# Optimization experiments

Hardware: AMD Instinct MI355X
Metric: run time of the kernel (lower is better)

## Reference

```python
import jax, jax.numpy as jnp
import numpy as np

N, IN_DIM, HID, OUT, E = 20000, 1024, 512, 128, 160000


def _xavier(key, fan_out, fan_in):
    a = (6.0 / (fan_in + fan_out)) ** 0.5
    return jax.random.uniform(key, (fan_out, fan_in), jnp.float32, -a, a)


def setup_inputs() -> dict:
    key = jax.random.key(0)
    ks = jax.random.split(key, 8)
    features = jax.random.normal(ks[0], (N, IN_DIM), jnp.float32)
    edge_index = jax.random.randint(ks[1], (2, E), 0, N, jnp.int64)
    W1 = _xavier(ks[2], HID, IN_DIM)   # conv1.lin.weight [out,in]
    b1 = jnp.zeros((HID,), jnp.float32)
    W2 = _xavier(ks[3], OUT, HID)      # conv2.lin.weight
    b2 = jnp.zeros((OUT,), jnp.float32)
    b3 = jnp.zeros((HID,), jnp.float32)  # conv3 bias (weight tied = W2.T)
    b4 = jnp.zeros((IN_DIM,), jnp.float32)  # conv4 bias (weight tied = W1.T)
    head1 = _xavier(ks[4], OUT, OUT)
    return dict(features=features, edge_index=edge_index, W1=W1, b1=b1,
                W2=W2, b2=b2, b3=b3, b4=b4, head1=head1)


def _gcn_conv(x, W, b, src, dst, norm, n):
    # GCNConv: transform then symmetric-normalized neighbor aggregation
    h = x @ W.T                       # [N, out]
    msg = h[src] * norm[:, None]      # [E', out] gathered + scaled
    out = jax.ops.segment_sum(msg, dst, num_segments=n)
    return out + b


def reference(features, edge_index, W1, b1, W2, b2, b3, b4, head1):
    n = features.shape[0]
    loops = jnp.arange(n, dtype=edge_index.dtype)
    src = jnp.concatenate([edge_index[0], loops])  # add self-loops
    dst = jnp.concatenate([edge_index[1], loops])
    deg = jax.ops.segment_sum(jnp.ones_like(dst, dtype=features.dtype), dst,
                              num_segments=n)
    dinv = jnp.where(deg > 0, deg ** -0.5, 0.0)
    norm = dinv[src] * dinv[dst]

    h1 = _gcn_conv(features, W1, b1, src, dst, norm, n)
    h2 = _gcn_conv(h1, W2, b2, src, dst, norm, n)
    z = h2 @ head1
    # tied weights: conv3.W = W2^T, conv4.W = W1^T
    h3 = _gcn_conv(z, W2.T, b3, src, dst, norm, n)
    h4 = _gcn_conv(h3, W1.T, b4, src, dst, norm, n)
    return z, h2, h4
```

## Files before the change

kernel.cpp:

```cpp
#include <hip/hip_runtime.h>

typedef short   short8  __attribute__((ext_vector_type(8)));
typedef unsigned short ushort8 __attribute__((ext_vector_type(8)));
typedef unsigned short bf4     __attribute__((ext_vector_type(4)));
typedef float   floatx4 __attribute__((ext_vector_type(4)));

__device__ __forceinline__ float bf2f(unsigned short h) {
    unsigned int u = ((unsigned int)h) << 16;
    return __builtin_bit_cast(float, u);
}
__device__ __forceinline__ unsigned short f2bf(float f) {
    unsigned int u = __builtin_bit_cast(unsigned int, f);
    u += 0x7fffu + ((u >> 16) & 1u);
    return (unsigned short)(u >> 16);
}


__global__ __launch_bounds__(256) void k_detect_f32(const unsigned short* __restrict__ X,
                                                    int nPairs, int* __restrict__ flags) {
    int i = blockIdx.x * 256 + threadIdx.x;
    if (i < nPairs) {
        unsigned short w = X[2 * i];
        if ((w & 0x7F80u) == 0x7F80u) atomicOr(&flags[0], 1);
    }
}

__global__ __launch_bounds__(256) void k_detect_i32(const int* __restrict__ ei,
                                                    int E, int* __restrict__ flags) {
    int i = blockIdx.x * 256 + threadIdx.x;
    if (i < E) {
        if (ei[2 * i + 1] != 0) atomicOr(&flags[1], 1);
    }
}


__global__ __launch_bounds__(256) void k_cvt_f32(const void* __restrict__ in,
                                                 float* __restrict__ out, int n,
                                                 const int* __restrict__ flags) {
    int i = blockIdx.x * 256 + threadIdx.x;
    if (i < n)
        out[i] = flags[0] ? ((const float*)in)[i] : bf2f(((const unsigned short*)in)[i]);
}

__global__ __launch_bounds__(256) void k_cvt8(const void* __restrict__ in,
                                              unsigned short* __restrict__ out,
                                              long n8, const int* __restrict__ flags) {
    long i = (long)blockIdx.x * 256 + threadIdx.x;
    if (i >= n8) return;
    ushort8 o;
    if (flags[0]) {
        const floatx4* f = (const floatx4*)in + i * 2;
        floatx4 a = f[0], b = f[1];
#pragma unroll
        for (int j = 0; j < 4; j++) { o[j] = f2bf(a[j]); o[4 + j] = f2bf(b[j]); }
    } else {
        o = *((const ushort8*)in + i);
    }
    *((ushort8*)out + i) = o;
}

__global__ __launch_bounds__(256) void k_tcvt(const void* __restrict__ in,
                                              unsigned short* __restrict__ out,
                                              int R, int C, const int* __restrict__ flags) {
    int idx = blockIdx.x * 256 + threadIdx.x;
    if (idx >= R * C) return;
    int r = idx / C, c = idx - r * C;
    unsigned short v = flags[0] ? f2bf(((const float*)in)[idx])
                                : ((const unsigned short*)in)[idx];
    out[(long)c * R + r] = v;
}


__global__ __launch_bounds__(256) void k_count(const int* __restrict__ ei, int E, int n,
                                               const int* __restrict__ flags,
                                               int* __restrict__ deg) {
    int e = blockIdx.x * 256 + threadIdx.x;
    if (e >= E) return;
    int sh = (flags[1] == 0) ? 1 : 0;
    int d = ei[(long)(E + e) << sh];
    if ((unsigned)d < (unsigned)n) atomicAdd(&deg[d], 1);
}

__global__ __launch_bounds__(256) void k_dinv(const int* __restrict__ deg,
                                              float* __restrict__ dinv, int n) {
    int i = blockIdx.x * 256 + threadIdx.x;
    if (i < n) dinv[i] = rsqrtf((float)(deg[i] + 1));
}

__global__ __launch_bounds__(1024) void k_scan(const int* __restrict__ deg,
                                               int* __restrict__ row_start,
                                               int* __restrict__ cursor, int n) {
    __shared__ int sums[1024];
    int t = threadIdx.x;
    int CH = (n + 1 + 1023) / 1024;
    int base = t * CH;
    int s = 0;
    for (int i = 0; i < CH; i++) {
        int idx = base + i;
        if (idx < n) s += deg[idx];
    }
    sums[t] = s;
    __syncthreads();
    for (int off = 1; off < 1024; off <<= 1) {
        int v = (t >= off) ? sums[t - off] : 0;
        __syncthreads();
        if (t >= off) sums[t] += v;
        __syncthreads();
    }
    int run = (t > 0) ? sums[t - 1] : 0;
    for (int i = 0; i < CH; i++) {
        int idx = base + i;
        if (idx < n) {
            row_start[idx] = run;
            cursor[idx] = run;
            run += deg[idx];
        } else if (idx == n) {
            row_start[n] = run;
        }
    }
}

__global__ __launch_bounds__(256) void k_fill(const int* __restrict__ ei, int E, int n,
                                              const int* __restrict__ flags,
                                              int* __restrict__ cursor,
                                              int* __restrict__ csr) {
    int e = blockIdx.x * 256 + threadIdx.x;
    if (e >= E) return;
    int sh = (flags[1] == 0) ? 1 : 0;
    int s = ei[(long)e << sh];
    int d = ei[(long)(E + e) << sh];
    if ((unsigned)d >= (unsigned)n || (unsigned)s >= (unsigned)n) return;
    int p = atomicAdd(&cursor[d], 1);
    csr[p] = s;
}


template <int BM, int BN>
__global__ __launch_bounds__(256, (BN == 128 ? 3 : 4))
void gemm_nt(const unsigned short* __restrict__ A,
             const unsigned short* __restrict__ Bt,
             void* __restrict__ Cv, long coff,
             const float* __restrict__ bias,
             int M, int N, int K, int finalOut,
             const int* __restrict__ flags) {
    constexpr int BK = 32, LDT = 40;
    constexpr int JR = BN / 16;
    constexpr int SM = BM / 64;
    __shared__ unsigned short sA[2][BM * LDT];
    __shared__ unsigned short sB[2][BN * LDT];
    const bool of32 = finalOut && flags[0];
    const bool hasb = bias != nullptr;
    const int t = threadIdx.x;

    const int GX = gridDim.x;
    const int nwg = GX * gridDim.y;
    const int orig = blockIdx.y * GX + blockIdx.x;
    const int q8 = nwg >> 3, r8 = nwg & 7;
    const int xcd = orig & 7, cidx = orig >> 3;
    const int swz = (xcd < r8 ? xcd * (q8 + 1) : r8 * (q8 + 1) + (xcd - r8) * q8) + cidx;
    const int m0 = (swz / GX) * BM;
    const int n0 = (swz % GX) * BN;

    const int w = t >> 6;
    const int lane = t & 63;
    const int id = lane & 15;
    const int q = lane >> 4;

    floatx4 acc[SM][JR];
#pragma unroll
    for (int s = 0; s < SM; s++)
#pragma unroll
        for (int j = 0; j < JR; j++) acc[s][j] = (floatx4)0.0f;

    const int ar = t >> 2;
    const int ac = (t & 3) * 8;

    const unsigned short* pa0 = A + (long)min(m0 + ar, M - 1) * K + ac;
    const unsigned short* pa1 = (SM == 2)
        ? A + (long)min(m0 + ar + 64, M - 1) * K + ac : pa0;
    const unsigned short* pb0 = Bt + (long)min(n0 + ar, N - 1) * K + ac;
    const unsigned short* pb1 = (JR == 8)
        ? Bt + (long)min(n0 + ar + 64, N - 1) * K + ac : pb0;

    {
        ushort8 va0 = *(const ushort8*)(pa0);
        ushort8 va1; if (SM == 2) va1 = *(const ushort8*)(pa1);
        ushort8 vb0 = *(const ushort8*)(pb0);
        ushort8 vb1; if (JR == 8) vb1 = *(const ushort8*)(pb1);
        *(ushort8*)(sA[0] + ar * LDT + ac) = va0;
        if (SM == 2) *(ushort8*)(sA[0] + (ar + 64) * LDT + ac) = va1;
        *(ushort8*)(sB[0] + ar * LDT + ac) = vb0;
        if (JR == 8) *(ushort8*)(sB[0] + (ar + 64) * LDT + ac) = vb1;
        __syncthreads();
    }

    auto STEP = [&](int k0, const unsigned short* sAr, const unsigned short* sBr,
                    unsigned short* sAw, unsigned short* sBw, bool last) {
        ushort8 na0, na1, nb0, nb1;
        if (!last) {
            na0 = *(const ushort8*)(pa0 + k0 + BK);
            if (SM == 2) na1 = *(const ushort8*)(pa1 + k0 + BK);
            nb0 = *(const ushort8*)(pb0 + k0 + BK);
            if (JR == 8) nb1 = *(const ushort8*)(pb1 + k0 + BK);
        }
        short8 afrag[SM], bfrag[JR];
#pragma unroll
        for (int s = 0; s < SM; s++)
            afrag[s] = *(const short8*)(sAr + ((SM == 2 ? 32 * w + 16 * s : 16 * w) + id) * LDT + q * 8);
#pragma unroll
        for (int j = 0; j < JR; j++)
            bfrag[j] = *(const short8*)(sBr + (16 * j + id) * LDT + q * 8);
#pragma unroll
        for (int s = 0; s < SM; s++)
#pragma unroll
            for (int j = 0; j < JR; j++)
                acc[s][j] = __builtin_amdgcn_mfma_f32_16x16x32_bf16(
                    bfrag[j], afrag[s], acc[s][j], 0, 0, 0);
        if (!last) {
            *(ushort8*)(sAw + ar * LDT + ac) = na0;
            if (SM == 2) *(ushort8*)(sAw + (ar + 64) * LDT + ac) = na1;
            *(ushort8*)(sBw + ar * LDT + ac) = nb0;
            if (JR == 8) *(ushort8*)(sBw + (ar + 64) * LDT + ac) = nb1;
            __syncthreads();
        }
    };

    for (int k0 = 0; k0 < K; k0 += 2 * BK) {
        STEP(k0, sA[0], sB[0], sA[1], sB[1], false);
        STEP(k0 + BK, sA[1], sB[1], sA[0], sB[0], k0 + 2 * BK >= K);
    }

#pragma unroll
    for (int s = 0; s < SM; s++) {
        const int row = m0 + (SM == 2 ? 32 * w + 16 * s : 16 * w) + id;
        if (row < M) {
#pragma unroll
            for (int j = 0; j < JR; j++) {
                const int colb = n0 + 16 * j + 4 * q;
                floatx4 v = acc[s][j];
                if (hasb) v = v + *(const floatx4*)(bias + colb);
                const long off = coff + (long)row * N + colb;
                if (of32) {
                    *(floatx4*)((float*)Cv + off) = v;
                } else {
                    bf4 o;
#pragma unroll
                    for (int r = 0; r < 4; r++) o[r] = f2bf(v[r]);
                    *(bf4*)((unsigned short*)Cv + off) = o;
                }
            }
        }
    }
}


template <int D>
__global__ __launch_bounds__(256) void k_agg(const unsigned short* __restrict__ T,
                                             const int* __restrict__ rs,
                                             const int* __restrict__ csr,
                                             const float* __restrict__ dinv,
                                             const float* __restrict__ bias,
                                             unsigned short* __restrict__ O, int n) {
    constexpr int TPN = D / 8;
    constexpr int NPB = 256 / TPN;
    int lt = threadIdx.x % TPN;
    int node = blockIdx.x * NPB + threadIdx.x / TPN;
    if (node >= n) return;
    int off = lt * 8;
    float acc[8];
#pragma unroll
    for (int i = 0; i < 8; i++) acc[i] = 0.0f;
    int beg = rs[node], end = rs[node + 1];
    for (int j = beg; j < end; j++) {
        int s = csr[j];
        if ((unsigned)s >= (unsigned)n) continue;
        float wgt = dinv[s];
        ushort8 v = *(const ushort8*)(T + (long)s * D + off);
#pragma unroll
        for (int i = 0; i < 8; i++) acc[i] += wgt * bf2f(v[i]);
    }
    float di = dinv[node];
    ushort8 sv = *(const ushort8*)(T + (long)node * D + off);
    ushort8 o;
#pragma unroll
    for (int i = 0; i < 8; i++) {
        float r = di * (acc[i] + di * bf2f(sv[i])) + (bias ? bias[off + i] : 0.0f);
        o[i] = f2bf(r);
    }
    *(ushort8*)(O + (long)node * D + off) = o;
}


__global__ __launch_bounds__(256) void k_out(const unsigned short* __restrict__ z,
                                             const unsigned short* __restrict__ h2,
                                             void* __restrict__ out, int nOut,
                                             const int* __restrict__ flags) {
    int i = blockIdx.x * 256 + threadIdx.x;
    if (i >= 2 * nOut) return;
    unsigned short v = (i < nOut) ? z[i] : h2[i - nOut];
    if (flags[0]) ((float*)out)[i] = bf2f(v);
    else ((unsigned short*)out)[i] = v;
}


extern "C" void kernel_launch(void* const* d_in, const int* in_sizes, int n_in,
                              void* d_out, int out_size, void* d_ws, size_t ws_size,
                              hipStream_t stream) {
    const int IN  = in_sizes[7];
    const int HID = in_sizes[3];
    const int OUT = in_sizes[5];
    const int Nn  = in_sizes[0] / IN;
    const int E   = in_sizes[1] / 2;

    const void* X   = d_in[0];
    const int*  ei  = (const int*)d_in[1];
    const void* W1  = d_in[2];
    const void* b1  = d_in[3];
    const void* W2  = d_in[4];
    const void* b2  = d_in[5];
    const void* b3  = d_in[6];
    const void* b4  = d_in[7];
    const void* Hd1 = d_in[8];

    char* base = (char*)d_ws;
    size_t o = 0;
    auto carve = [&](size_t bytes) -> char* {
        char* p = base + o;
        o = (o + bytes + 255) & ~(size_t)255;
        return p;
    };
    int*   flags  = (int*)carve(2 * 4);
    int*   deg    = (int*)carve((size_t)Nn * 4);
    int*   rowst  = (int*)carve((size_t)(Nn + 1) * 4);
    int*   cursor = (int*)carve((size_t)Nn * 4);
    float* dinv   = (float*)carve((size_t)Nn * 4);
    int*   csr    = (int*)carve((size_t)E * 4);
    float* biasf  = (float*)carve((size_t)(HID + OUT + HID + IN) * 4);
    float* bc1 = biasf, *bc2 = biasf + HID, *bc3 = biasf + HID + OUT,
         *bc4 = biasf + HID + OUT + HID;
    unsigned short* W1t  = (unsigned short*)carve((size_t)IN * HID * 2);
    unsigned short* W2t  = (unsigned short*)carve((size_t)HID * OUT * 2);
    unsigned short* H1t  = (unsigned short*)carve((size_t)OUT * OUT * 2);
    unsigned short* W1c  = (unsigned short*)carve((size_t)HID * IN * 2);
    unsigned short* W2c  = (unsigned short*)carve((size_t)OUT * HID * 2);
    unsigned short* Xb   = (unsigned short*)carve((size_t)Nn * IN * 2);
    unsigned short* t1   = (unsigned short*)carve((size_t)Nn * HID * 2);
    unsigned short* h1   = (unsigned short*)carve((size_t)Nn * HID * 2);
    unsigned short* h3   = (unsigned short*)carve((size_t)Nn * HID * 2);
    unsigned short* t2   = (unsigned short*)carve((size_t)Nn * OUT * 2);
    unsigned short* h2ws = (unsigned short*)carve((size_t)Nn * OUT * 2);
    unsigned short* zws  = (unsigned short*)carve((size_t)Nn * OUT * 2);

    hipMemsetAsync(flags, 0, 8, stream);
    hipMemsetAsync(deg, 0, (size_t)Nn * 4, stream);
    int nPairs = 1 << 20;
    k_detect_f32<<<(nPairs + 255) / 256, 256, 0, stream>>>((const unsigned short*)X, nPairs, flags);
    k_detect_i32<<<(E + 255) / 256, 256, 0, stream>>>(ei, E, flags);

    k_cvt_f32<<<(HID + 255) / 256, 256, 0, stream>>>(b1, bc1, HID, flags);
    k_cvt_f32<<<(OUT + 255) / 256, 256, 0, stream>>>(b2, bc2, OUT, flags);
    k_cvt_f32<<<(HID + 255) / 256, 256, 0, stream>>>(b3, bc3, HID, flags);
    k_cvt_f32<<<(IN + 255) / 256, 256, 0, stream>>>(b4, bc4, IN, flags);

    k_tcvt<<<(HID * IN + 255) / 256, 256, 0, stream>>>(W1, W1t, HID, IN, flags);
    k_tcvt<<<(OUT * HID + 255) / 256, 256, 0, stream>>>(W2, W2t, OUT, HID, flags);
    k_tcvt<<<(OUT * OUT + 255) / 256, 256, 0, stream>>>(Hd1, H1t, OUT, OUT, flags);

    {
        long n8x = (long)Nn * IN / 8;
        k_cvt8<<<(int)((n8x + 255) / 256), 256, 0, stream>>>(X, Xb, n8x, flags);
        long n8w1 = (long)HID * IN / 8;
        k_cvt8<<<(int)((n8w1 + 255) / 256), 256, 0, stream>>>(W1, W1c, n8w1, flags);
        long n8w2 = (long)OUT * HID / 8;
        k_cvt8<<<(int)((n8w2 + 255) / 256), 256, 0, stream>>>(W2, W2c, n8w2, flags);
    }

    k_count<<<(E + 255) / 256, 256, 0, stream>>>(ei, E, Nn, flags, deg);
    k_dinv<<<(Nn + 255) / 256, 256, 0, stream>>>(deg, dinv, Nn);
    k_scan<<<1, 1024, 0, stream>>>(deg, rowst, cursor, Nn);
    k_fill<<<(E + 255) / 256, 256, 0, stream>>>(ei, E, Nn, flags, cursor, csr);

    dim3 blk(256);
    auto ggrid = [&](int Ncols, int bn, int bm) {
        return dim3((Ncols + bn - 1) / bn, (Nn + bm - 1) / bm);
    };
    const long h2Off = (long)Nn * OUT, h4Off = (long)Nn * OUT * 2;

    gemm_nt<128, 64><<<ggrid(HID, 64, 128), blk, 0, stream>>>(Xb, W1c, t1, 0, nullptr, Nn, HID, IN, 0, flags);
    k_agg<512><<<(Nn * 64 + 255) / 256, blk, 0, stream>>>(t1, rowst, csr, dinv, bc1, h1, Nn);

    gemm_nt<64, 64><<<ggrid(OUT, 64, 64), blk, 0, stream>>>(h1, W2c, t2, 0, nullptr, Nn, OUT, HID, 0, flags);
    k_agg<128><<<(Nn * 16 + 255) / 256, blk, 0, stream>>>(t2, rowst, csr, dinv, bc2, h2ws, Nn);

    gemm_nt<64, 64><<<ggrid(OUT, 64, 64), blk, 0, stream>>>(h2ws, H1t, zws, 0, nullptr, Nn, OUT, OUT, 0, flags);

    k_agg<128><<<(Nn * 16 + 255) / 256, blk, 0, stream>>>(zws, rowst, csr, dinv, nullptr, t2, Nn);
    gemm_nt<128, 64><<<ggrid(HID, 64, 128), blk, 0, stream>>>(t2, W2t, h3, 0, bc3, Nn, HID, OUT, 0, flags);

    k_agg<512><<<(Nn * 64 + 255) / 256, blk, 0, stream>>>(h3, rowst, csr, dinv, nullptr, t1, Nn);
    gemm_nt<128, 128><<<ggrid(IN, 128, 128), blk, 0, stream>>>(t1, W1t, d_out, h4Off, bc4, Nn, IN, HID, 1, flags);

    k_out<<<(2 * (int)h2Off + 255) / 256, blk, 0, stream>>>(zws, h2ws, d_out, (int)h2Off, flags);
}
```

Baseline: 546.0 us.

## Fuse input conversions into GEMM loads and outputs into producers; merge prologue kernels

The first GEMMs now read fp32 inputs directly and convert them to bf16 while staging into shared memory, so the separate full-matrix conversion of the features (20000x1024) and of W1/W2 is no longer needed. The z and h2 outputs are written straight from the GEMM and aggregation epilogues, which removes the final copy kernel. Detection, degree zeroing and the bias conversions are merged into fewer launches, and the weight transpose now goes through tiled shared memory. The cost is twice the global traffic per A tile in the first GEMM, plus extra branches and registers in the GEMM loop.

```diff
diff --git a/kernel.cpp b/kernel.cpp
--- a/kernel.cpp
+++ b/kernel.cpp
@@ -16,58 +16,65 @@
 }
 
 
-__global__ __launch_bounds__(256) void k_detect_f32(const unsigned short* __restrict__ X,
-                                                    int nPairs, int* __restrict__ flags) {
+__global__ __launch_bounds__(256) void k_detect(const unsigned short* __restrict__ X,
+                                                int nPairs, const int* __restrict__ ei,
+                                                int E, int n,
+                                                int* __restrict__ flags,
+                                                int* __restrict__ deg) {
     int i = blockIdx.x * 256 + threadIdx.x;
     if (i < nPairs) {
         unsigned short w = X[2 * i];
         if ((w & 0x7F80u) == 0x7F80u) atomicOr(&flags[0], 1);
     }
-}
-
-__global__ __launch_bounds__(256) void k_detect_i32(const int* __restrict__ ei,
-                                                    int E, int* __restrict__ flags) {
-    int i = blockIdx.x * 256 + threadIdx.x;
     if (i < E) {
         if (ei[2 * i + 1] != 0) atomicOr(&flags[1], 1);
     }
-}
-
-
-__global__ __launch_bounds__(256) void k_cvt_f32(const void* __restrict__ in,
-                                                 float* __restrict__ out, int n,
-                                                 const int* __restrict__ flags) {
+    if (i < n) deg[i] = 0;
+}
+
+
+__global__ __launch_bounds__(256) void k_cvtb(const void* __restrict__ b1,
+                                              const void* __restrict__ b2,
+                                              const void* __restrict__ b3,
+                                              const void* __restrict__ b4,
+                                              float* __restrict__ out,
+                                              int L1, int L2, int L3, int L4,
+                                              const int* __restrict__ flags) {
     int i = blockIdx.x * 256 + threadIdx.x;
-    if (i < n)
-        out[i] = flags[0] ? ((const float*)in)[i] : bf2f(((const unsigned short*)in)[i]);
-}
-
-__global__ __launch_bounds__(256) void k_cvt8(const void* __restrict__ in,
-                                              unsigned short* __restrict__ out,
-                                              long n8, const int* __restrict__ flags) {
-    long i = (long)blockIdx.x * 256 + threadIdx.x;
-    if (i >= n8) return;
-    ushort8 o;
-    if (flags[0]) {
-        const floatx4* f = (const floatx4*)in + i * 2;
-        floatx4 a = f[0], b = f[1];
-#pragma unroll
-        for (int j = 0; j < 4; j++) { o[j] = f2bf(a[j]); o[4 + j] = f2bf(b[j]); }
-    } else {
-        o = *((const ushort8*)in + i);
-    }
-    *((ushort8*)out + i) = o;
-}
+    int n = L1 + L2 + L3 + L4;
+    if (i >= n) return;
+    const void* src; int off;
+    if (i < L1)                { src = b1; off = i; }
+    else if (i < L1 + L2)      { src = b2; off = i - L1; }
+    else if (i < L1 + L2 + L3) { src = b3; off = i - L1 - L2; }
+    else                       { src = b4; off = i - L1 - L2 - L3; }
+    out[i] = flags[0] ? ((const float*)src)[off]
+                      : bf2f(((const unsigned short*)src)[off]);
+}
+
 
 __global__ __launch_bounds__(256) void k_tcvt(const void* __restrict__ in,
                                               unsigned short* __restrict__ out,
                                               int R, int C, const int* __restrict__ flags) {
-    int idx = blockIdx.x * 256 + threadIdx.x;
-    if (idx >= R * C) return;
-    int r = idx / C, c = idx - r * C;
-    unsigned short v = flags[0] ? f2bf(((const float*)in)[idx])
-                                : ((const unsigned short*)in)[idx];
-    out[(long)c * R + r] = v;
+    __shared__ unsigned short tl[32][40];
+    const int c0 = blockIdx.x * 32, r0 = blockIdx.y * 32;
+    const int tx = threadIdx.x & 31, ty = threadIdx.x >> 5;
+    const bool f32 = flags[0] != 0;
+#pragma unroll
+    for (int k = 0; k < 32; k += 8) {
+        int r = r0 + ty + k, c = c0 + tx;
+        unsigned short v = 0;
+        if (r < R && c < C)
+            v = f32 ? f2bf(((const float*)in)[(long)r * C + c])
+                    : ((const unsigned short*)in)[(long)r * C + c];
+        tl[ty + k][tx] = v;
+    }
+    __syncthreads();
+#pragma unroll
+    for (int k = 0; k < 32; k += 8) {
+        int c = c0 + ty + k, r = r0 + tx;
+        if (c < C && r < R) out[(long)c * R + r] = tl[tx][ty + k];
+    }
 }
 
 
@@ -135,11 +142,29 @@
 }
 
 
+__device__ __forceinline__ void ld_any(const void* base, long elem, bool f32,
+                                       ushort8& u, floatx4& f0, floatx4& f1) {
+    if (f32) {
+        const floatx4* p = (const floatx4*)((const float*)base + elem);
+        f0 = p[0]; f1 = p[1];
+    } else {
+        u = *(const ushort8*)((const unsigned short*)base + elem);
+    }
+}
+__device__ __forceinline__ ushort8 cv_any(bool f32, ushort8 u, floatx4 f0, floatx4 f1) {
+    if (!f32) return u;
+    ushort8 r;
+#pragma unroll
+    for (int j = 0; j < 4; j++) { r[j] = f2bf(f0[j]); r[4 + j] = f2bf(f1[j]); }
+    return r;
+}
+
 template <int BM, int BN>
 __global__ __launch_bounds__(256, (BN == 128 ? 3 : 4))
-void gemm_nt(const unsigned short* __restrict__ A,
-             const unsigned short* __restrict__ Bt,
+void gemm_nt(const void* __restrict__ A, int aMaybeF32,
+             const void* __restrict__ Bt, int bMaybeF32,
              void* __restrict__ Cv, long coff,
+             void* __restrict__ Cv2, long c2off,
              const float* __restrict__ bias,
              int M, int N, int K, int finalOut,
              const int* __restrict__ flags) {
@@ -148,7 +173,10 @@
     constexpr int SM = BM / 64;
     __shared__ unsigned short sA[2][BM * LDT];
     __shared__ unsigned short sB[2][BN * LDT];
-    const bool of32 = finalOut && flags[0];
+    const bool isf32 = flags[0] != 0;
+    const bool af32 = aMaybeF32 && isf32;
+    const bool bf32 = bMaybeF32 && isf32;
+    const bool of32 = finalOut && isf32;
     const bool hasb = bias != nullptr;
     const int t = threadIdx.x;
 
@@ -175,33 +203,37 @@
     const int ar = t >> 2;
     const int ac = (t & 3) * 8;
 
-    const unsigned short* pa0 = A + (long)min(m0 + ar, M - 1) * K + ac;
-    const unsigned short* pa1 = (SM == 2)
-        ? A + (long)min(m0 + ar + 64, M - 1) * K + ac : pa0;
-    const unsigned short* pb0 = Bt + (long)min(n0 + ar, N - 1) * K + ac;
-    const unsigned short* pb1 = (JR == 8)
-        ? Bt + (long)min(n0 + ar + 64, N - 1) * K + ac : pb0;
+    const long ea0 = (long)min(m0 + ar, M - 1) * K + ac;
+    const long ea1 = (SM == 2) ? (long)min(m0 + ar + 64, M - 1) * K + ac : ea0;
+    const long eb0 = (long)min(n0 + ar, N - 1) * K + ac;
+    const long eb1 = (JR == 8) ? (long)min(n0 + ar + 64, N - 1) * K + ac : eb0;
 
     {
-        ushort8 va0 = *(const ushort8*)(pa0);
-        ushort8 va1; if (SM == 2) va1 = *(const ushort8*)(pa1);
-        ushort8 vb0 = *(const ushort8*)(pb0);
-        ushort8 vb1; if (JR == 8) vb1 = *(const ushort8*)(pb1);
-        *(ushort8*)(sA[0] + ar * LDT + ac) = va0;
-        if (SM == 2) *(ushort8*)(sA[0] + (ar + 64) * LDT + ac) = va1;
-        *(ushort8*)(sB[0] + ar * LDT + ac) = vb0;
-        if (JR == 8) *(ushort8*)(sB[0] + (ar + 64) * LDT + ac) = vb1;
+        ushort8 u; floatx4 f0, f1;
+        ld_any(A, ea0, af32, u, f0, f1);
+        *(ushort8*)(sA[0] + ar * LDT + ac) = cv_any(af32, u, f0, f1);
+        if (SM == 2) {
+            ld_any(A, ea1, af32, u, f0, f1);
+            *(ushort8*)(sA[0] + (ar + 64) * LDT + ac) = cv_any(af32, u, f0, f1);
+        }
+        ld_any(Bt, eb0, bf32, u, f0, f1);
+        *(ushort8*)(sB[0] + ar * LDT + ac) = cv_any(bf32, u, f0, f1);
+        if (JR == 8) {
+            ld_any(Bt, eb1, bf32, u, f0, f1);
+            *(ushort8*)(sB[0] + (ar + 64) * LDT + ac) = cv_any(bf32, u, f0, f1);
+        }
         __syncthreads();
     }
 
     auto STEP = [&](int k0, const unsigned short* sAr, const unsigned short* sBr,
                     unsigned short* sAw, unsigned short* sBw, bool last) {
         ushort8 na0, na1, nb0, nb1;
+        floatx4 fa00, fa01, fa10, fa11, fb00, fb01, fb10, fb11;
         if (!last) {
-            na0 = *(const ushort8*)(pa0 + k0 + BK);
-            if (SM == 2) na1 = *(const ushort8*)(pa1 + k0 + BK);
-            nb0 = *(const ushort8*)(pb0 + k0 + BK);
-            if (JR == 8) nb1 = *(const ushort8*)(pb1 + k0 + BK);
+            ld_any(A, ea0 + k0 + BK, af32, na0, fa00, fa01);
+            if (SM == 2) ld_any(A, ea1 + k0 + BK, af32, na1, fa10, fa11);
+            ld_any(Bt, eb0 + k0 + BK, bf32, nb0, fb00, fb01);
+            if (JR == 8) ld_any(Bt, eb1 + k0 + BK, bf32, nb1, fb10, fb11);
         }
         short8 afrag[SM], bfrag[JR];
 #pragma unroll
@@ -217,10 +249,10 @@
                 acc[s][j] = __builtin_amdgcn_mfma_f32_16x16x32_bf16(
                     bfrag[j], afrag[s], acc[s][j], 0, 0, 0);
         if (!last) {
-            *(ushort8*)(sAw + ar * LDT + ac) = na0;
-            if (SM == 2) *(ushort8*)(sAw + (ar + 64) * LDT + ac) = na1;
-            *(ushort8*)(sBw + ar * LDT + ac) = nb0;
-            if (JR == 8) *(ushort8*)(sBw + (ar + 64) * LDT + ac) = nb1;
+            *(ushort8*)(sAw + ar * LDT + ac) = cv_any(af32, na0, fa00, fa01);
+            if (SM == 2) *(ushort8*)(sAw + (ar + 64) * LDT + ac) = cv_any(af32, na1, fa10, fa11);
+            *(ushort8*)(sBw + ar * LDT + ac) = cv_any(bf32, nb0, fb00, fb01);
+            if (JR == 8) *(ushort8*)(sBw + (ar + 64) * LDT + ac) = cv_any(bf32, nb1, fb10, fb11);
             __syncthreads();
         }
     };
@@ -248,6 +280,17 @@
                     for (int r = 0; r < 4; r++) o[r] = f2bf(v[r]);
                     *(bf4*)((unsigned short*)Cv + off) = o;
                 }
+                if (Cv2) {
+                    const long off2 = c2off + (long)row * N + colb;
+                    if (isf32) {
+                        *(floatx4*)((float*)Cv2 + off2) = v;
+                    } else {
+                        bf4 o;
+#pragma unroll
+                        for (int r = 0; r < 4; r++) o[r] = f2bf(v[r]);
+                        *(bf4*)((unsigned short*)Cv2 + off2) = o;
+                    }
+                }
             }
         }
     }
@@ -260,7 +303,9 @@
                                              const int* __restrict__ csr,
                                              const float* __restrict__ dinv,
                                              const float* __restrict__ bias,
-                                             unsigned short* __restrict__ O, int n) {
+                                             unsigned short* __restrict__ O,
+                                             void* __restrict__ O2, long o2off,
+                                             const int* __restrict__ flags, int n) {
     constexpr int TPN = D / 8;
     constexpr int NPB = 256 / TPN;
     int lt = threadIdx.x % TPN;
@@ -281,25 +326,27 @@
     }
     float di = dinv[node];
     ushort8 sv = *(const ushort8*)(T + (long)node * D + off);
+    float res[8];
     ushort8 o;
 #pragma unroll
     for (int i = 0; i < 8; i++) {
-        float r = di * (acc[i] + di * bf2f(sv[i])) + (bias ? bias[off + i] : 0.0f);
-        o[i] = f2bf(r);
+        res[i] = di * (acc[i] + di * bf2f(sv[i])) + (bias ? bias[off + i] : 0.0f);
+        o[i] = f2bf(res[i]);
     }
     *(ushort8*)(O + (long)node * D + off) = o;
-}
-
-
-__global__ __launch_bounds__(256) void k_out(const unsigned short* __restrict__ z,
-                                             const unsigned short* __restrict__ h2,
-                                             void* __restrict__ out, int nOut,
-                                             const int* __restrict__ flags) {
-    int i = blockIdx.x * 256 + threadIdx.x;
-    if (i >= 2 * nOut) return;
-    unsigned short v = (i < nOut) ? z[i] : h2[i - nOut];
-    if (flags[0]) ((float*)out)[i] = bf2f(v);
-    else ((unsigned short*)out)[i] = v;
+    if (O2) {
+        const long p = o2off + (long)node * D + off;
+        if (flags[0]) {
+            float* dst = (float*)O2 + p;
+            floatx4 v0, v1;
+#pragma unroll
+            for (int i = 0; i < 4; i++) { v0[i] = res[i]; v1[i] = res[4 + i]; }
+            *(floatx4*)(dst) = v0;
+            *(floatx4*)(dst + 4) = v1;
+        } else {
+            *(ushort8*)((unsigned short*)O2 + p) = o;
+        }
+    }
 }
 
 
@@ -341,9 +388,6 @@
     unsigned short* W1t  = (unsigned short*)carve((size_t)IN * HID * 2);
     unsigned short* W2t  = (unsigned short*)carve((size_t)HID * OUT * 2);
     unsigned short* H1t  = (unsigned short*)carve((size_t)OUT * OUT * 2);
-    unsigned short* W1c  = (unsigned short*)carve((size_t)HID * IN * 2);
-    unsigned short* W2c  = (unsigned short*)carve((size_t)OUT * HID * 2);
-    unsigned short* Xb   = (unsigned short*)carve((size_t)Nn * IN * 2);
     unsigned short* t1   = (unsigned short*)carve((size_t)Nn * HID * 2);
     unsigned short* h1   = (unsigned short*)carve((size_t)Nn * HID * 2);
     unsigned short* h3   = (unsigned short*)carve((size_t)Nn * HID * 2);
@@ -352,28 +396,19 @@
     unsigned short* zws  = (unsigned short*)carve((size_t)Nn * OUT * 2);
 
     hipMemsetAsync(flags, 0, 8, stream);
-    hipMemsetAsync(deg, 0, (size_t)Nn * 4, stream);
     int nPairs = 1 << 20;
-    k_detect_f32<<<(nPairs + 255) / 256, 256, 0, stream>>>((const unsigned short*)X, nPairs, flags);
-    k_detect_i32<<<(E + 255) / 256, 256, 0, stream>>>(ei, E, flags);
-
-    k_cvt_f32<<<(HID + 255) / 256, 256, 0, stream>>>(b1, bc1, HID, flags);
-    k_cvt_f32<<<(OUT + 255) / 256, 256, 0, stream>>>(b2, bc2, OUT, flags);
-    k_cvt_f32<<<(HID + 255) / 256, 256, 0, stream>>>(b3, bc3, HID, flags);
-    k_cvt_f32<<<(IN + 255) / 256, 256, 0, stream>>>(b4, bc4, IN, flags);
-
-    k_tcvt<<<(HID * IN + 255) / 256, 256, 0, stream>>>(W1, W1t, HID, IN, flags);
-    k_tcvt<<<(OUT * HID + 255) / 256, 256, 0, stream>>>(W2, W2t, OUT, HID, flags);
-    k_tcvt<<<(OUT * OUT + 255) / 256, 256, 0, stream>>>(Hd1, H1t, OUT, OUT, flags);
-
     {
-        long n8x = (long)Nn * IN / 8;
-        k_cvt8<<<(int)((n8x + 255) / 256), 256, 0, stream>>>(X, Xb, n8x, flags);
-        long n8w1 = (long)HID * IN / 8;
-        k_cvt8<<<(int)((n8w1 + 255) / 256), 256, 0, stream>>>(W1, W1c, n8w1, flags);
-        long n8w2 = (long)OUT * HID / 8;
-        k_cvt8<<<(int)((n8w2 + 255) / 256), 256, 0, stream>>>(W2, W2c, n8w2, flags);
-    }
+        int gmax = nPairs;
+        k_detect<<<(gmax + 255) / 256, 256, 0, stream>>>(
+            (const unsigned short*)X, nPairs, ei, E, Nn, flags, deg);
+    }
+
+    k_cvtb<<<(HID + OUT + HID + IN + 255) / 256, 256, 0, stream>>>(
+        b1, b2, b3, b4, biasf, HID, OUT, HID, IN, flags);
+
+    k_tcvt<<<dim3((IN + 31) / 32, (HID + 31) / 32), 256, 0, stream>>>(W1, W1t, HID, IN, flags);
+    k_tcvt<<<dim3((HID + 31) / 32, (OUT + 31) / 32), 256, 0, stream>>>(W2, W2t, OUT, HID, flags);
+    k_tcvt<<<dim3((OUT + 31) / 32, (OUT + 31) / 32), 256, 0, stream>>>(Hd1, H1t, OUT, OUT, flags);
 
     k_count<<<(E + 255) / 256, 256, 0, stream>>>(ei, E, Nn, flags, deg);
     k_dinv<<<(Nn + 255) / 256, 256, 0, stream>>>(deg, dinv, Nn);
@@ -386,19 +421,26 @@
     };
     const long h2Off = (long)Nn * OUT, h4Off = (long)Nn * OUT * 2;
 
-    gemm_nt<128, 64><<<ggrid(HID, 64, 128), blk, 0, stream>>>(Xb, W1c, t1, 0, nullptr, Nn, HID, IN, 0, flags);
-    k_agg<512><<<(Nn * 64 + 255) / 256, blk, 0, stream>>>(t1, rowst, csr, dinv, bc1, h1, Nn);
-
-    gemm_nt<64, 64><<<ggrid(OUT, 64, 64), blk, 0, stream>>>(h1, W2c, t2, 0, nullptr, Nn, OUT, HID, 0, flags);
-    k_agg<128><<<(Nn * 16 + 255) / 256, blk, 0, stream>>>(t2, rowst, csr, dinv, bc2, h2ws, Nn);
-
-    gemm_nt<64, 64><<<ggrid(OUT, 64, 64), blk, 0, stream>>>(h2ws, H1t, zws, 0, nullptr, Nn, OUT, OUT, 0, flags);
-
-    k_agg<128><<<(Nn * 16 + 255) / 256, blk, 0, stream>>>(zws, rowst, csr, dinv, nullptr, t2, Nn);
-    gemm_nt<128, 64><<<ggrid(HID, 64, 128), blk, 0, stream>>>(t2, W2t, h3, 0, bc3, Nn, HID, OUT, 0, flags);
-
-    k_agg<512><<<(Nn * 64 + 255) / 256, blk, 0, stream>>>(h3, rowst, csr, dinv, nullptr, t1, Nn);
-    gemm_nt<128, 128><<<ggrid(IN, 128, 128), blk, 0, stream>>>(t1, W1t, d_out, h4Off, bc4, Nn, IN, HID, 1, flags);
-
-    k_out<<<(2 * (int)h2Off + 255) / 256, blk, 0, stream>>>(zws, h2ws, d_out, (int)h2Off, flags);
-}
+    gemm_nt<128, 64><<<ggrid(HID, 64, 128), blk, 0, stream>>>(
+        X, 1, W1, 1, t1, 0, nullptr, 0, nullptr, Nn, HID, IN, 0, flags);
+    k_agg<512><<<(Nn * 64 + 255) / 256, blk, 0, stream>>>(
+        t1, rowst, csr, dinv, bc1, h1, nullptr, 0, flags, Nn);
+
+    gemm_nt<64, 64><<<ggrid(OUT, 64, 64), blk, 0, stream>>>(
+        h1, 0, W2, 1, t2, 0, nullptr, 0, nullptr, Nn, OUT, HID, 0, flags);
+    k_agg<128><<<(Nn * 16 + 255) / 256, blk, 0, stream>>>(
+        t2, rowst, csr, dinv, bc2, h2ws, d_out, h2Off, flags, Nn);
+
+    gemm_nt<64, 64><<<ggrid(OUT, 64, 64), blk, 0, stream>>>(
+        h2ws, 0, H1t, 0, zws, 0, d_out, 0, nullptr, Nn, OUT, OUT, 0, flags);
+
+    k_agg<128><<<(Nn * 16 + 255) / 256, blk, 0, stream>>>(
+        zws, rowst, csr, dinv, nullptr, t2, nullptr, 0, flags, Nn);
+    gemm_nt<128, 64><<<ggrid(HID, 64, 128), blk, 0, stream>>>(
+        t2, 0, W2t, 0, h3, 0, nullptr, 0, bc3, Nn, HID, OUT, 0, flags);
+
+    k_agg<512><<<(Nn * 64 + 255) / 256, blk, 0, stream>>>(
+        h3, rowst, csr, dinv, nullptr, t1, nullptr, 0, flags, Nn);
+    gemm_nt<128, 128><<<ggrid(IN, 128, 128), blk, 0, stream>>>(
+        t1, 0, W1t, 0, d_out, h4Off, nullptr, 0, bc4, Nn, IN, HID, 1, flags);
+}
```

Result: slower. 611.0 us (+11.9%).
